# Optimization experiments

Hardware: AMD Instinct MI355X
Metric: run time of the kernel (lower is better)

## Reference

```python
import jax, jax.numpy as jnp
import numpy as np


def hard_sigmoid(x):
    # Keras hard_sigmoid: clip(0.2*x + 0.5, 0, 1)
    return jnp.clip(0.2 * x + 0.5, 0.0, 1.0)


def lstm_layer(x, W, U, b):
    """Run a Keras-style LSTM cell over time.

    x: [B, T, D], W: [D, 4H], U: [H, 4H], b: [4H]. Gate order i,f,g,o.
    Returns full hidden sequence [B, T, H].
    """
    B = x.shape[0]
    H = U.shape[0]
    h0 = jnp.zeros((B, H), dtype=x.dtype)
    c0 = jnp.zeros((B, H), dtype=x.dtype)
    # Precompute input projections for all timesteps in one big GEMM.
    xz = jnp.einsum('btd,dk->btk', x, W) + b  # [B, T, 4H]
    xz_t = jnp.swapaxes(xz, 0, 1)             # [T, B, 4H]

    def step(carry, zx_t):
        h, c = carry
        z = zx_t + h @ U                       # [B, 4H]
        i, f, g, o = jnp.split(z, 4, axis=-1)
        i = hard_sigmoid(i)
        f = hard_sigmoid(f)
        g = jnp.tanh(g)
        o = hard_sigmoid(o)
        c = f * c + i * g
        h = o * jnp.tanh(c)
        return (h, c), h

    (_, _), hs = jax.lax.scan(step, (h0, c0), xz_t)  # hs: [T, B, H]
    return jnp.swapaxes(hs, 0, 1)  # [B, T, H]


def setup_inputs() -> dict:
    key = jax.random.key(0)
    ks = jax.random.split(key, 7)
    B, T, D, H = 32, 512, 1024, 1024
    s_in = 1.0 / np.sqrt(D)
    s_h = 1.0 / np.sqrt(H)
    return {
        'x': jax.random.normal(ks[0], (B, T, D), dtype=jnp.float32),
        'W0': jax.random.normal(ks[1], (D, 4 * H), dtype=jnp.float32) * s_in,
        'U0': jax.random.normal(ks[2], (H, 4 * H), dtype=jnp.float32) * s_h,
        'b0': jnp.zeros((4 * H,), dtype=jnp.float32),
        'W1': jax.random.normal(ks[3], (H, 4 * H), dtype=jnp.float32) * s_h,
        'U1': jax.random.normal(ks[4], (H, 4 * H), dtype=jnp.float32) * s_h,
        'b1': jnp.zeros((4 * H,), dtype=jnp.float32),
    }


def reference(x, W0, U0, b0, W1, U1, b1):
    # StackedRNNCells: output of cell 0 at time t feeds cell 1 at time t.
    # Equivalent to running layer 0 over the whole sequence, then layer 1.
    h1 = lstm_layer(x, W0, U0, b0)    # [B, T, H]
    h2 = lstm_layer(h1, W1, U1, b1)   # [B, T, H]
    # RNN(return_sequences=False): last timestep output of the top cell.
    return h2[:, -1, :]
```

## Files before the change

### kernel.cpp

```cpp
#include <hip/hip_runtime.h>
#include <math.h>

#define B_  32
#define T_  512
#define H_  1024
#define G4_ 4096
#define NT  512
#define ROWP 1032
#define WROW 264

typedef __attribute__((ext_vector_type(8))) _Float16 f16x8;
typedef __attribute__((ext_vector_type(4))) float   f32x4;

__device__ __forceinline__ float hardsig(float z) {
    return fminf(fmaxf(0.2f * z + 0.5f, 0.0f), 1.0f);
}
__device__ __forceinline__ float fast_tanh(float x) {
    float ax = fabsf(x);
    float e  = __expf(-2.0f * ax);
    float t  = (1.0f - e) / (1.0f + e);
    return copysignf(t, x);
}
__device__ __forceinline__ unsigned ldA(const unsigned* p) {
    return __hip_atomic_load(p, __ATOMIC_RELAXED, __HIP_MEMORY_SCOPE_AGENT);
}
__device__ __forceinline__ void stA32(unsigned* p, unsigned v) {
    __hip_atomic_store(p, v, __ATOMIC_RELAXED, __HIP_MEMORY_SCOPE_AGENT);
}
__device__ __forceinline__ unsigned long long ldA64(const void* p) {
    return __hip_atomic_load((const unsigned long long*)p, __ATOMIC_RELAXED, __HIP_MEMORY_SCOPE_AGENT);
}
__device__ __forceinline__ void stA64(void* p, unsigned long long v) {
    __hip_atomic_store((unsigned long long*)p, v, __ATOMIC_RELAXED, __HIP_MEMORY_SCOPE_AGENT);
}
__device__ __forceinline__ float f16bits_to_f(unsigned short us) {
    _Float16 hf; __builtin_memcpy(&hf, &us, 2);
    return (float)hf;
}
__device__ __forceinline__ unsigned umin2(unsigned a, unsigned b) { return a < b ? a : b; }

__device__ __forceinline__ void load_wfrags(const float* M, int colbase, int myrow,
                                            int koff, bool keep, f16x8* wf, _Float16* st) {
    for (int kc = 0; kc < 4; ++kc) {
        __syncthreads();
        #pragma unroll
        for (int it = 0; it < 4; ++it) {
            int id  = it * NT + (int)threadIdx.x;
            int kl  = id >> 3, gc8 = id & 7;
            int gcol = (gc8 >> 1) * 1024 + colbase + (gc8 & 1) * 8;
            const float* src = M + (size_t)(kc * 256 + kl) * G4_ + gcol;
            float4 v0 = *(const float4*)src;
            float4 v1 = *(const float4*)(src + 4);
            int rb = gc8 * 8;
            st[(rb+0)*WROW+kl]=(_Float16)v0.x; st[(rb+1)*WROW+kl]=(_Float16)v0.y;
            st[(rb+2)*WROW+kl]=(_Float16)v0.z; st[(rb+3)*WROW+kl]=(_Float16)v0.w;
            st[(rb+4)*WROW+kl]=(_Float16)v1.x; st[(rb+5)*WROW+kl]=(_Float16)v1.y;
            st[(rb+6)*WROW+kl]=(_Float16)v1.z; st[(rb+7)*WROW+kl]=(_Float16)v1.w;
        }
        __syncthreads();
        if (keep) {
            #pragma unroll
            for (int kj = 0; kj < 8; ++kj)
                wf[kc*8+kj] = *(const f16x8*)&st[myrow * WROW + kj * 32 + koff];
        }
    }
    __syncthreads();
}


__global__ __launch_bounds__(NT, 1)
void lstm12(const float* __restrict__ x,
            const float* __restrict__ W0, const float* __restrict__ U0, const float* __restrict__ b0,
            const float* __restrict__ W1, const float* __restrict__ U1, const float* __restrict__ b1,
            _Float16* __restrict__ h1,
            _Float16* __restrict__ h2,
            _Float16* __restrict__ xzr,
            const _Float16* __restrict__ zp,
            unsigned* __restrict__ ctr,
            float* __restrict__ out)
{
    __shared__ __align__(16) char smem[149504];

    const int tid = threadIdx.x, bid = blockIdx.x;
    const int w = tid >> 6, l = tid & 63;
    const int koff = (l >> 4) * 8;

    if (bid >= 128) {
        _Float16* Wl = (_Float16*)smem;
        const int e = bid - 128, gbase = e * 64;
        for (int fi = tid; fi < 16384; fi += NT) {
            const int k = fi >> 4, rem = fi & 15;
            const float* src = W0 + (size_t)k * G4_ + gbase + rem * 4;
            float4 v = *(const float4*)src;
            const int kiG = k >> 5, jsub = 16 * ((k & 31) >> 3), e8 = k & 7;
            #pragma unroll
            for (int c = 0; c < 4; ++c) {
                const int j = rem * 4 + c, nf = j >> 4, lane = (j & 15) + jsub;
                float fv = (c == 0) ? v.x : (c == 1) ? v.y : (c == 2) ? v.z : v.w;
                Wl[((nf * 32 + kiG) * 64 + lane) * 8 + e8] = (_Float16)fv;
            }
        }
        float bb0[4];
        #pragma unroll
        for (int nf = 0; nf < 4; ++nf) bb0[nf] = b0[gbase + nf * 16 + (l & 15)];
        __syncthreads();

        for (int c = 0; c < 64; ++c) {
            if (c >= 4) {
                if (w == 0) {
                    const unsigned need = (unsigned)(8 * c - 24);
                    while (true) {
                        unsigned v = umin2(ldA(&ctr[2 * l]), ldA(&ctr[2 * l + 1]));
                        if (__all((int)(v >= need))) break;
                        __builtin_amdgcn_s_sleep(1);
                    }
                }
                __syncthreads();
            }

            f32x4 acc[2][4];
            #pragma unroll
            for (int p = 0; p < 2; ++p)
                #pragma unroll
                for (int nf = 0; nf < 4; ++nf) acc[p][nf] = (f32x4){0.f, 0.f, 0.f, 0.f};
            const float* xrow[2];
            #pragma unroll
            for (int p = 0; p < 2; ++p) {
                const int m = (w * 2 + p) * 16 + (l & 15);
                xrow[p] = x + ((size_t)(m & 31) * T_ + (8 * c + (m >> 5))) * 1024;
            }
            #pragma unroll 4
            for (int kiG = 0; kiG < 32; ++kiG) {
                const int kk = kiG * 32 + koff;
                f16x8 af[2];
                #pragma unroll
                for (int p = 0; p < 2; ++p) {
                    float4 v0 = *(const float4*)&xrow[p][kk];
                    float4 v1 = *(const float4*)&xrow[p][kk + 4];
                    af[p][0]=(_Float16)v0.x; af[p][1]=(_Float16)v0.y;
                    af[p][2]=(_Float16)v0.z; af[p][3]=(_Float16)v0.w;
                    af[p][4]=(_Float16)v1.x; af[p][5]=(_Float16)v1.y;
                    af[p][6]=(_Float16)v1.z; af[p][7]=(_Float16)v1.w;
                }
                #pragma unroll
                for (int nf = 0; nf < 4; ++nf) {
                    f16x8 bf = *(const f16x8*)&Wl[((nf * 32 + kiG) * 64 + l) * 8];
                    acc[0][nf] = __builtin_amdgcn_mfma_f32_16x16x32_f16(af[0], bf, acc[0][nf], 0, 0, 0);
                    acc[1][nf] = __builtin_amdgcn_mfma_f32_16x16x32_f16(af[1], bf, acc[1][nf], 0, 0, 0);
                }
            }
            #pragma unroll
            for (int p = 0; p < 2; ++p)
                #pragma unroll
                for (int nf = 0; nf < 4; ++nf)
                    #pragma unroll
                    for (int i = 0; i < 4; ++i) {
                        _Float16 hf = (_Float16)(acc[p][nf][i] + bb0[nf]);
                        unsigned short us; __builtin_memcpy(&us, &hf, 2);
                        unsigned up = us;
                        unsigned op = (unsigned)__shfl_xor((int)up, 1);
                        if (!(l & 1)) {
                            const int m = (w * 2 + p) * 16 + (l >> 4) * 4 + i;
                            size_t off = (((size_t)(c & 3) * 8 + (m >> 5)) * B_ + (m & 31)) * G4_
                                       + gbase + nf * 16 + ((l & 15) & ~1);
                            stA32((unsigned*)&xzr[off], up | (op << 16));
                        }
                    }
            asm volatile("s_waitcnt vmcnt(0)" ::: "memory");
            __syncthreads();
            if (tid == 0) stA32(&ctr[384 + e], (unsigned)(c + 1));
        }
        return;
    }

    const int dom = (bid >= 64);
    const int db  = bid & 63;
    const int jb  = db * 16;

    _Float16* stA = (_Float16*)smem;
    _Float16* stB = (_Float16*)(smem + 66048);
    float*    red = (float*)(smem + (dom ? 132096 : 66048));
    #define RED(slot, row, col) red[((slot) * 16 + (row)) * 17 + (col)]

    f16x8 wf[32];
    const int gq = w & 3;
    const int myrow = gq * 16 + (l & 15);
    if (dom == 0) {
        load_wfrags(U0, jb, myrow, koff, true, wf, stA);
    } else {
        const int rl = w >> 2;
        load_wfrags(W1, jb, myrow, koff, (rl == 0), wf, stA);
        load_wfrags(U1, jb, myrow, koff, (rl == 1), wf, stA);
    }

    const int cidx = w * 64 + l;
    const int cb = cidx >> 2, j4 = (cidx & 3) * 4;
    float creg[4] = {0.f, 0.f, 0.f, 0.f};
    float bias_[4][4];
    if (dom == 1 && w < 2) {
        #pragma unroll
        for (int g = 0; g < 4; ++g)
            #pragma unroll
            for (int c = 0; c < 4; ++c)
                bias_[g][c] = b1[(size_t)g * H_ + jb + j4 + c];
    }
    const int mt = w >> 2;
    const int rl = w >> 2;

    for (int t = 0; t < T_; ++t) {
        if (w == 0) {
            if (dom == 0) {
                const unsigned xt = (unsigned)((t >> 3) + 1);
                while (true) {
                    bool ok = (ldA(&ctr[384 + l]) >= xt);
                    if (t > 0) {
                        unsigned v0 = umin2(ldA(&ctr[2 * l]), ldA(&ctr[2 * l + 1]));
                        ok = ok && (v0 >= (unsigned)t);
                    }
                    if (__all((int)ok)) break;
                    __builtin_amdgcn_s_sleep(1);
                }
            } else {
                while (true) {
                    unsigned v0 = umin2(ldA(&ctr[2 * l]), ldA(&ctr[2 * l + 1]));
                    bool ok = (v0 >= (unsigned)(t + 1));
                    if (t > 0) {
                        unsigned v1 = umin2(ldA(&ctr[128 + 2 * l]), ldA(&ctr[128 + 2 * l + 1]));
                        ok = ok && (v1 >= (unsigned)t);
                    }
                    if (__all((int)ok)) break;
                    __builtin_amdgcn_s_sleep(1);
                }
            }
        }
        __syncthreads();

        if (dom == 0) {
            const char* src = t ? (const char*)(h1 + (size_t)(t - 1) * B_ * H_) : (const char*)zp;
            #pragma unroll
            for (int it = 0; it < 8; ++it) {
                const int fb = tid * 16 + it * 8192;
                const int row = fb >> 11, rb = fb & 2047;
                *(uint4*)&smem[row * 2064 + rb] = *(const uint4*)(src + fb);
            }
        } else {
            const char* s1 = (const char*)(h1 + (size_t)t * B_ * H_);
            const char* s2 = t ? (const char*)(h2 + (size_t)(t - 1) * B_ * H_) : (const char*)zp;
            #pragma unroll
            for (int it = 0; it < 8; ++it) {
                const int fb = tid * 16 + it * 8192;
                const int row = fb >> 11, rb = fb & 2047;
                *(uint4*)&smem[row * 2064 + rb] = *(const uint4*)(s1 + fb);
                *(uint4*)&smem[66048 + row * 2064 + rb] = *(const uint4*)(s2 + fb);
            }
        }
        unsigned long long xzq[4];
        if (dom == 0 && w < 2) {
            const size_t xbase = (((size_t)((t >> 3) & 3) * 8 + (t & 7)) * B_ + cb) * G4_ + jb + j4;
            #pragma unroll
            for (int gg = 0; gg < 4; ++gg) xzq[gg] = ldA64(&xzr[xbase + gg * 1024]);
        }
        __syncthreads();

        if (dom == 0) {
            const _Float16* ar = stA + (mt * 16 + (l & 15)) * ROWP;
            f32x4 ac0 = {0,0,0,0}, ac1 = {0,0,0,0}, ac2 = {0,0,0,0}, ac3 = {0,0,0,0};
            #pragma unroll
            for (int k = 0; k < 32; k += 4) {
                ac0 = __builtin_amdgcn_mfma_f32_16x16x32_f16(*(const f16x8*)&ar[(k+0)*32 + koff], wf[k+0], ac0, 0, 0, 0);
                ac1 = __builtin_amdgcn_mfma_f32_16x16x32_f16(*(const f16x8*)&ar[(k+1)*32 + koff], wf[k+1], ac1, 0, 0, 0);
                ac2 = __builtin_amdgcn_mfma_f32_16x16x32_f16(*(const f16x8*)&ar[(k+2)*32 + koff], wf[k+2], ac2, 0, 0, 0);
                ac3 = __builtin_amdgcn_mfma_f32_16x16x32_f16(*(const f16x8*)&ar[(k+3)*32 + koff], wf[k+3], ac3, 0, 0, 0);
            }
            f32x4 acc = (ac0 + ac1) + (ac2 + ac3);
            #pragma unroll
            for (int i = 0; i < 4; ++i)
                RED(mt * 4 + gq, (l >> 4) * 4 + i, (l & 15)) = acc[i];
        } else {
            const _Float16* ab = (rl ? stB : stA);
            const _Float16* ar0 = ab + (l & 15) * ROWP;
            const _Float16* ar1 = ab + (16 + (l & 15)) * ROWP;
            f32x4 ac0 = {0,0,0,0}, ac1 = {0,0,0,0};
            #pragma unroll
            for (int k = 0; k < 32; ++k) {
                const int kk = k * 32 + koff;
                f16x8 bfr = wf[k];
                ac0 = __builtin_amdgcn_mfma_f32_16x16x32_f16(*(const f16x8*)&ar0[kk], bfr, ac0, 0, 0, 0);
                ac1 = __builtin_amdgcn_mfma_f32_16x16x32_f16(*(const f16x8*)&ar1[kk], bfr, ac1, 0, 0, 0);
            }
            #pragma unroll
            for (int i = 0; i < 4; ++i) {
                RED(rl * 8 + 0 * 4 + gq, (l >> 4) * 4 + i, (l & 15)) = ac0[i];
                RED(rl * 8 + 1 * 4 + gq, (l >> 4) * 4 + i, (l & 15)) = ac1[i];
            }
        }
        __syncthreads();

        if (w < 2) {
            const int rmt = cb >> 4, row = cb & 15;
            unsigned long long pk = 0;
            float hv4[4];
            if (dom == 0) {
                asm volatile("s_waitcnt vmcnt(0)" ::: "memory");
                #pragma unroll
                for (int c = 0; c < 4; ++c) {
                    float z[4];
                    #pragma unroll
                    for (int gg = 0; gg < 4; ++gg) {
                        float xv = f16bits_to_f((unsigned short)((xzq[gg] >> (16 * c)) & 0xffffu));
                        z[gg] = RED(rmt * 4 + gg, row, j4 + c) + xv;
                    }
                    float ig = hardsig(z[0]), fg = hardsig(z[1]);
                    float gv = fast_tanh(z[2]), og = hardsig(z[3]);
                    creg[c] = fg * creg[c] + ig * gv;
                    hv4[c] = og * fast_tanh(creg[c]);
                    _Float16 hf = (_Float16)hv4[c];
                    unsigned short us; __builtin_memcpy(&us, &hf, 2);
                    pk |= ((unsigned long long)us) << (16 * c);
                }
                stA64(&h1[((size_t)t * B_ + cb) * H_ + jb + j4], pk);
                asm volatile("s_waitcnt vmcnt(0)" ::: "memory");
                if (l == 0) stA32(&ctr[db * 2 + w], (unsigned)(t + 1));
            } else {
                #pragma unroll
                for (int c = 0; c < 4; ++c) {
                    float z[4];
                    #pragma unroll
                    for (int gg = 0; gg < 4; ++gg)
                        z[gg] = RED(0 + rmt * 4 + gg, row, j4 + c)
                              + RED(8 + rmt * 4 + gg, row, j4 + c) + bias_[gg][c];
                    float ig = hardsig(z[0]), fg = hardsig(z[1]);
                    float gv = fast_tanh(z[2]), og = hardsig(z[3]);
                    creg[c] = fg * creg[c] + ig * gv;
                    hv4[c] = og * fast_tanh(creg[c]);
                    _Float16 hf = (_Float16)hv4[c];
                    unsigned short us; __builtin_memcpy(&us, &hf, 2);
                    pk |= ((unsigned long long)us) << (16 * c);
                }
                stA64(&h2[((size_t)t * B_ + cb) * H_ + jb + j4], pk);
                if (t == T_ - 1)
                    *(float4*)&out[(size_t)cb * H_ + jb + j4] = make_float4(hv4[0], hv4[1], hv4[2], hv4[3]);
                asm volatile("s_waitcnt vmcnt(0)" ::: "memory");
                if (l == 0) stA32(&ctr[128 + db * 2 + w], (unsigned)(t + 1));
            }
        }
    }
}

extern "C" void kernel_launch(void* const* d_in, const int* in_sizes, int n_in,
                              void* d_out, int out_size, void* d_ws, size_t ws_size,
                              hipStream_t stream) {
    const float* x  = (const float*)d_in[0];
    const float* W0 = (const float*)d_in[1];
    const float* U0 = (const float*)d_in[2];
    const float* b0 = (const float*)d_in[3];
    const float* W1 = (const float*)d_in[4];
    const float* U1 = (const float*)d_in[5];
    const float* b1 = (const float*)d_in[6];
    float* out = (float*)d_out;

    char* ws = (char*)d_ws;
    const size_t off_h1 = 0;
    const size_t off_h2 = 33554432;
    const size_t off_xz = 67108864;
    const size_t off_zp = 75497472;
    const size_t off_ct = 75563008;

    _Float16* h1  = (_Float16*)(ws + off_h1);
    _Float16* h2  = (_Float16*)(ws + off_h2);
    _Float16* xzr = (_Float16*)(ws + off_xz);
    _Float16* zp  = (_Float16*)(ws + off_zp);
    unsigned* ctr = (unsigned*)(ws + off_ct);

    hipMemsetAsync(ws + off_zp, 0, 65536 + 8192, stream);

    hipLaunchKernelGGL(lstm12, dim3(192), dim3(NT), 0, stream,
                       x, W0, U0, b0, W1, U1, b1,
                       h1, h2, xzr, zp, ctr, out);
}
```

Measured before the change: 4.195 ms.

## Replace per-step counter barriers with sentinel-polled data flags for hidden-state handoff

Instead of having each block spin on per-timestep counters before loading the previous hidden state, the h1/h2 buffers are pre-filled with 0xFF sentinels. Consumers poll the data itself until no sentinel words remain and stage it into LDS. Layer-0 counters are now published only every 8 steps, and layer-1 counters are dropped entirely. This removes a global flag round trip and the extra s_waitcnt from the recurrence critical path. The cost is a 64MB memset each call and relying on 32-bit halves of valid fp16 data never equalling 0xFFFFFFFF (a pair of fp16 NaNs).

```diff
diff --git a/kernel.cpp b/kernel.cpp
--- a/kernel.cpp
+++ b/kernel.cpp
@@ -8,6 +8,7 @@
 #define NT  512
 #define ROWP 1032
 #define WROW 264
+#define SENT 0xFFFFFFFFu
 
 typedef __attribute__((ext_vector_type(8))) _Float16 f16x8;
 typedef __attribute__((ext_vector_type(4))) float   f32x4;
@@ -38,6 +39,38 @@
     return (float)hf;
 }
 __device__ __forceinline__ unsigned umin2(unsigned a, unsigned b) { return a < b ? a : b; }
+
+__device__ __forceinline__ void stage_poll(const char* src, char* dst, int tid) {
+    unsigned long long a[8], b[8];
+    #pragma unroll
+    for (int it = 0; it < 8; ++it) {
+        const char* p = src + tid * 16 + it * 8192;
+        a[it] = ldA64(p); b[it] = ldA64(p + 8);
+    }
+    unsigned pend = 0xFFu;
+    while (true) {
+        unsigned np = 0;
+        #pragma unroll
+        for (int it = 0; it < 8; ++it)
+            if (pend & (1u << it))
+                if ((unsigned)a[it] == SENT || (unsigned)b[it] == SENT) np |= (1u << it);
+        #pragma unroll
+        for (int it = 0; it < 8; ++it)
+            if ((pend & (1u << it)) && !(np & (1u << it))) {
+                const int fb = tid * 16 + it * 8192;
+                unsigned long long* d = (unsigned long long*)(dst + (fb >> 11) * 2064 + (fb & 2047));
+                d[0] = a[it]; d[1] = b[it];
+            }
+        pend = np;
+        if (!pend) break;
+        #pragma unroll
+        for (int it = 0; it < 8; ++it)
+            if (pend & (1u << it)) {
+                const char* p = src + tid * 16 + it * 8192;
+                a[it] = ldA64(p); b[it] = ldA64(p + 8);
+            }
+    }
+}
 
 __device__ __forceinline__ void load_wfrags(const float* M, int colbase, int myrow,
                                             int koff, bool keep, f16x8* wf, _Float16* st) {
@@ -69,7 +102,7 @@
 
 
 __global__ __launch_bounds__(NT, 1)
-void lstm12(const float* __restrict__ x,
+void lstm13(const float* __restrict__ x,
             const float* __restrict__ W0, const float* __restrict__ U0, const float* __restrict__ b0,
             const float* __restrict__ W1, const float* __restrict__ U1, const float* __restrict__ b1,
             _Float16* __restrict__ h1,
@@ -117,7 +150,6 @@
                 }
                 __syncthreads();
             }
-
             f32x4 acc[2][4];
             #pragma unroll
             for (int p = 0; p < 2; ++p)
@@ -178,7 +210,6 @@
     const int jb  = db * 16;
 
     _Float16* stA = (_Float16*)smem;
-    _Float16* stB = (_Float16*)(smem + 66048);
     float*    red = (float*)(smem + (dom ? 132096 : 66048));
     #define RED(slot, row, col) red[((slot) * 16 + (row)) * 17 + (col)]
 
@@ -188,9 +219,9 @@
     if (dom == 0) {
         load_wfrags(U0, jb, myrow, koff, true, wf, stA);
     } else {
-        const int rl = w >> 2;
-        load_wfrags(W1, jb, myrow, koff, (rl == 0), wf, stA);
-        load_wfrags(U1, jb, myrow, koff, (rl == 1), wf, stA);
+        const int rl0 = w >> 2;
+        load_wfrags(W1, jb, myrow, koff, (rl0 == 0), wf, stA);
+        load_wfrags(U1, jb, myrow, koff, (rl0 == 1), wf, stA);
     }
 
     const int cidx = w * 64 + l;
@@ -207,62 +238,23 @@
     const int mt = w >> 2;
     const int rl = w >> 2;
 
-    for (int t = 0; t < T_; ++t) {
-        if (w == 0) {
-            if (dom == 0) {
+    if (dom == 0) {
+        for (int t = 0; t < T_; ++t) {
+            if (w < 2 && (t & 7) == 0) {
                 const unsigned xt = (unsigned)((t >> 3) + 1);
-                while (true) {
-                    bool ok = (ldA(&ctr[384 + l]) >= xt);
-                    if (t > 0) {
-                        unsigned v0 = umin2(ldA(&ctr[2 * l]), ldA(&ctr[2 * l + 1]));
-                        ok = ok && (v0 >= (unsigned)t);
-                    }
-                    if (__all((int)ok)) break;
-                    __builtin_amdgcn_s_sleep(1);
-                }
-            } else {
-                while (true) {
-                    unsigned v0 = umin2(ldA(&ctr[2 * l]), ldA(&ctr[2 * l + 1]));
-                    bool ok = (v0 >= (unsigned)(t + 1));
-                    if (t > 0) {
-                        unsigned v1 = umin2(ldA(&ctr[128 + 2 * l]), ldA(&ctr[128 + 2 * l + 1]));
-                        ok = ok && (v1 >= (unsigned)t);
-                    }
-                    if (__all((int)ok)) break;
-                    __builtin_amdgcn_s_sleep(1);
-                }
-            }
-        }
-        __syncthreads();
-
-        if (dom == 0) {
+                while (!__all((int)(ldA(&ctr[384 + l]) >= xt))) __builtin_amdgcn_s_sleep(1);
+                asm volatile("" ::: "memory");
+            }
             const char* src = t ? (const char*)(h1 + (size_t)(t - 1) * B_ * H_) : (const char*)zp;
-            #pragma unroll
-            for (int it = 0; it < 8; ++it) {
-                const int fb = tid * 16 + it * 8192;
-                const int row = fb >> 11, rb = fb & 2047;
-                *(uint4*)&smem[row * 2064 + rb] = *(const uint4*)(src + fb);
-            }
-        } else {
-            const char* s1 = (const char*)(h1 + (size_t)t * B_ * H_);
-            const char* s2 = t ? (const char*)(h2 + (size_t)(t - 1) * B_ * H_) : (const char*)zp;
-            #pragma unroll
-            for (int it = 0; it < 8; ++it) {
-                const int fb = tid * 16 + it * 8192;
-                const int row = fb >> 11, rb = fb & 2047;
-                *(uint4*)&smem[row * 2064 + rb] = *(const uint4*)(s1 + fb);
-                *(uint4*)&smem[66048 + row * 2064 + rb] = *(const uint4*)(s2 + fb);
-            }
-        }
-        unsigned long long xzq[4];
-        if (dom == 0 && w < 2) {
-            const size_t xbase = (((size_t)((t >> 3) & 3) * 8 + (t & 7)) * B_ + cb) * G4_ + jb + j4;
-            #pragma unroll
-            for (int gg = 0; gg < 4; ++gg) xzq[gg] = ldA64(&xzr[xbase + gg * 1024]);
-        }
-        __syncthreads();
-
-        if (dom == 0) {
+            stage_poll(src, smem, tid);
+            unsigned long long xzq[4];
+            if (w < 2) {
+                const size_t xbase = (((size_t)((t >> 3) & 3) * 8 + (t & 7)) * B_ + cb) * G4_ + jb + j4;
+                #pragma unroll
+                for (int gg = 0; gg < 4; ++gg) xzq[gg] = ldA64(&xzr[xbase + gg * 1024]);
+            }
+            __syncthreads();
+
             const _Float16* ar = stA + (mt * 16 + (l & 15)) * ROWP;
             f32x4 ac0 = {0,0,0,0}, ac1 = {0,0,0,0}, ac2 = {0,0,0,0}, ac3 = {0,0,0,0};
             #pragma unroll
@@ -276,32 +268,12 @@
             #pragma unroll
             for (int i = 0; i < 4; ++i)
                 RED(mt * 4 + gq, (l >> 4) * 4 + i, (l & 15)) = acc[i];
-        } else {
-            const _Float16* ab = (rl ? stB : stA);
-            const _Float16* ar0 = ab + (l & 15) * ROWP;
-            const _Float16* ar1 = ab + (16 + (l & 15)) * ROWP;
-            f32x4 ac0 = {0,0,0,0}, ac1 = {0,0,0,0};
-            #pragma unroll
-            for (int k = 0; k < 32; ++k) {
-                const int kk = k * 32 + koff;
-                f16x8 bfr = wf[k];
-                ac0 = __builtin_amdgcn_mfma_f32_16x16x32_f16(*(const f16x8*)&ar0[kk], bfr, ac0, 0, 0, 0);
-                ac1 = __builtin_amdgcn_mfma_f32_16x16x32_f16(*(const f16x8*)&ar1[kk], bfr, ac1, 0, 0, 0);
-            }
-            #pragma unroll
-            for (int i = 0; i < 4; ++i) {
-                RED(rl * 8 + 0 * 4 + gq, (l >> 4) * 4 + i, (l & 15)) = ac0[i];
-                RED(rl * 8 + 1 * 4 + gq, (l >> 4) * 4 + i, (l & 15)) = ac1[i];
-            }
-        }
-        __syncthreads();
-
-        if (w < 2) {
-            const int rmt = cb >> 4, row = cb & 15;
-            unsigned long long pk = 0;
-            float hv4[4];
-            if (dom == 0) {
+            __syncthreads();
+
+            if (w < 2) {
                 asm volatile("s_waitcnt vmcnt(0)" ::: "memory");
+                const int rmt = cb >> 4, row = cb & 15;
+                unsigned long long pk = 0;
                 #pragma unroll
                 for (int c = 0; c < 4; ++c) {
                     float z[4];
@@ -313,15 +285,49 @@
                     float ig = hardsig(z[0]), fg = hardsig(z[1]);
                     float gv = fast_tanh(z[2]), og = hardsig(z[3]);
                     creg[c] = fg * creg[c] + ig * gv;
-                    hv4[c] = og * fast_tanh(creg[c]);
-                    _Float16 hf = (_Float16)hv4[c];
+                    float hv = og * fast_tanh(creg[c]);
+                    _Float16 hf = (_Float16)hv;
                     unsigned short us; __builtin_memcpy(&us, &hf, 2);
                     pk |= ((unsigned long long)us) << (16 * c);
                 }
                 stA64(&h1[((size_t)t * B_ + cb) * H_ + jb + j4], pk);
-                asm volatile("s_waitcnt vmcnt(0)" ::: "memory");
-                if (l == 0) stA32(&ctr[db * 2 + w], (unsigned)(t + 1));
-            } else {
+                if ((t & 7) == 7) {
+                    asm volatile("s_waitcnt vmcnt(0)" ::: "memory");
+                    if (l == 0) stA32(&ctr[db * 2 + w], (unsigned)(t + 1));
+                }
+            }
+        }
+    } else {
+        _Float16* stB = (_Float16*)(smem + 66048);
+        for (int t = 0; t < T_; ++t) {
+            const char* s2 = t ? (const char*)(h2 + (size_t)(t - 1) * B_ * H_) : (const char*)zp;
+            stage_poll(s2, (char*)stB, tid);
+            const char* s1 = (const char*)(h1 + (size_t)t * B_ * H_);
+            stage_poll(s1, smem, tid);
+            __syncthreads();
+
+            const _Float16* ab = (rl ? stB : stA);
+            const _Float16* ar0 = ab + (l & 15) * ROWP;
+            const _Float16* ar1 = ab + (16 + (l & 15)) * ROWP;
+            f32x4 ac0 = {0,0,0,0}, ac1 = {0,0,0,0};
+            #pragma unroll
+            for (int k = 0; k < 32; ++k) {
+                const int kk = k * 32 + koff;
+                f16x8 bfr = wf[k];
+                ac0 = __builtin_amdgcn_mfma_f32_16x16x32_f16(*(const f16x8*)&ar0[kk], bfr, ac0, 0, 0, 0);
+                ac1 = __builtin_amdgcn_mfma_f32_16x16x32_f16(*(const f16x8*)&ar1[kk], bfr, ac1, 0, 0, 0);
+            }
+            #pragma unroll
+            for (int i = 0; i < 4; ++i) {
+                RED(rl * 8 + 0 * 4 + gq, (l >> 4) * 4 + i, (l & 15)) = ac0[i];
+                RED(rl * 8 + 1 * 4 + gq, (l >> 4) * 4 + i, (l & 15)) = ac1[i];
+            }
+            __syncthreads();
+
+            if (w < 2) {
+                const int rmt = cb >> 4, row = cb & 15;
+                unsigned long long pk = 0;
+                float hv4[4];
                 #pragma unroll
                 for (int c = 0; c < 4; ++c) {
                     float z[4];
@@ -340,8 +346,6 @@
                 stA64(&h2[((size_t)t * B_ + cb) * H_ + jb + j4], pk);
                 if (t == T_ - 1)
                     *(float4*)&out[(size_t)cb * H_ + jb + j4] = make_float4(hv4[0], hv4[1], hv4[2], hv4[3]);
-                asm volatile("s_waitcnt vmcnt(0)" ::: "memory");
-                if (l == 0) stA32(&ctr[128 + db * 2 + w], (unsigned)(t + 1));
             }
         }
     }
@@ -372,9 +376,10 @@
     _Float16* zp  = (_Float16*)(ws + off_zp);
     unsigned* ctr = (unsigned*)(ws + off_ct);
 
+    hipMemsetAsync(ws, 0xFF, 67108864, stream);
     hipMemsetAsync(ws + off_zp, 0, 65536 + 8192, stream);
 
-    hipLaunchKernelGGL(lstm12, dim3(192), dim3(NT), 0, stream,
+    hipLaunchKernelGGL(lstm13, dim3(192), dim3(NT), 0, stream,
                        x, W0, U0, b0, W1, U1, b1,
                        h1, h2, xzr, zp, ctr, out);
 }
```

New measurement: 4.922 ms. 17.3% more time.

## Swizzle staged h tiles into MFMA fragment layout and split per-wave waits

Applied to the files above, without the earlier changes.

The hidden-state tile staged into LDS now uses an XOR-swizzled, fragment-ordered layout instead of padded rows. Each lane can then read its MFMA A operand with one contiguous 16-byte access, with fewer bank conflicts. The single wave-0 spin followed by __syncthreads is replaced by per-wave spins, so each wave group waits only on the counters for the data it stages. In layer 2, the two wave halves now stage h1 and h2 separately, which lets one half start loading before the other half's dependency is met. The dom-0 MFMA chain shrinks from four accumulators to two.

```diff
diff --git a/kernel.cpp b/kernel.cpp
--- a/kernel.cpp
+++ b/kernel.cpp
@@ -6,7 +6,6 @@
 #define H_  1024
 #define G4_ 4096
 #define NT  512
-#define ROWP 1032
 #define WROW 264
 
 typedef __attribute__((ext_vector_type(8))) _Float16 f16x8;
@@ -38,6 +37,15 @@
     return (float)hf;
 }
 __device__ __forceinline__ unsigned umin2(unsigned a, unsigned b) { return a < b ? a : b; }
+
+__device__ __forceinline__ void stage_granule(const char* src, _Float16* dst, int fb) {
+    uint4 v = *(const uint4*)(src + fb);
+    const int r = fb >> 11, c0 = (fb & 2047) >> 1;
+    const int kiG = c0 >> 5, q = (c0 >> 3) & 3;
+    const int ln = (r & 15) + 16 * q;
+    const int pl = ln ^ ((ln >> 3) & 6) ^ (kiG & 1);
+    *(uint4*)&dst[(((r >> 4) * 32 + kiG) * 64 + pl) * 8] = v;
+}
 
 __device__ __forceinline__ void load_wfrags(const float* M, int colbase, int myrow,
                                             int koff, bool keep, f16x8* wf, _Float16* st) {
@@ -69,7 +77,7 @@
 
 
 __global__ __launch_bounds__(NT, 1)
-void lstm12(const float* __restrict__ x,
+void lstm14(const float* __restrict__ x,
             const float* __restrict__ W0, const float* __restrict__ U0, const float* __restrict__ b0,
             const float* __restrict__ W1, const float* __restrict__ U1, const float* __restrict__ b1,
             _Float16* __restrict__ h1,
@@ -79,11 +87,12 @@
             unsigned* __restrict__ ctr,
             float* __restrict__ out)
 {
-    __shared__ __align__(16) char smem[149504];
+    __shared__ __align__(16) char smem[148480];
 
     const int tid = threadIdx.x, bid = blockIdx.x;
     const int w = tid >> 6, l = tid & 63;
     const int koff = (l >> 4) * 8;
+    const int pl0 = l ^ ((l >> 3) & 6);
 
     if (bid >= 128) {
         _Float16* Wl = (_Float16*)smem;
@@ -117,7 +126,6 @@
                 }
                 __syncthreads();
             }
-
             f32x4 acc[2][4];
             #pragma unroll
             for (int p = 0; p < 2; ++p)
@@ -178,8 +186,8 @@
     const int jb  = db * 16;
 
     _Float16* stA = (_Float16*)smem;
-    _Float16* stB = (_Float16*)(smem + 66048);
-    float*    red = (float*)(smem + (dom ? 132096 : 66048));
+    _Float16* stB = (_Float16*)(smem + 65536);
+    float*    red = (float*)(smem + (dom ? 131072 : 65536));
     #define RED(slot, row, col) red[((slot) * 16 + (row)) * 17 + (col)]
 
     f16x8 wf[32];
@@ -188,9 +196,9 @@
     if (dom == 0) {
         load_wfrags(U0, jb, myrow, koff, true, wf, stA);
     } else {
-        const int rl = w >> 2;
-        load_wfrags(W1, jb, myrow, koff, (rl == 0), wf, stA);
-        load_wfrags(U1, jb, myrow, koff, (rl == 1), wf, stA);
+        const int rl0 = w >> 2;
+        load_wfrags(W1, jb, myrow, koff, (rl0 == 0), wf, stA);
+        load_wfrags(U1, jb, myrow, koff, (rl0 == 1), wf, stA);
     }
 
     const int cidx = w * 64 + l;
@@ -206,53 +214,51 @@
     }
     const int mt = w >> 2;
     const int rl = w >> 2;
+    const int wr = w & 3;
 
     for (int t = 0; t < T_; ++t) {
-        if (w == 0) {
-            if (dom == 0) {
-                const unsigned xt = (unsigned)((t >> 3) + 1);
-                while (true) {
-                    bool ok = (ldA(&ctr[384 + l]) >= xt);
-                    if (t > 0) {
-                        unsigned v0 = umin2(ldA(&ctr[2 * l]), ldA(&ctr[2 * l + 1]));
-                        ok = ok && (v0 >= (unsigned)t);
-                    }
-                    if (__all((int)ok)) break;
-                    __builtin_amdgcn_s_sleep(1);
-                }
-            } else {
+        if (dom == 0) {
+            if (t > 0) {
                 while (true) {
                     unsigned v0 = umin2(ldA(&ctr[2 * l]), ldA(&ctr[2 * l + 1]));
-                    bool ok = (v0 >= (unsigned)(t + 1));
-                    if (t > 0) {
-                        unsigned v1 = umin2(ldA(&ctr[128 + 2 * l]), ldA(&ctr[128 + 2 * l + 1]));
-                        ok = ok && (v1 >= (unsigned)t);
-                    }
-                    if (__all((int)ok)) break;
+                    if (__all((int)(v0 >= (unsigned)t))) break;
                     __builtin_amdgcn_s_sleep(1);
                 }
             }
-        }
-        __syncthreads();
+            if (w < 2) {
+                const unsigned xt = (unsigned)((t >> 3) + 1);
+                while (!__all((int)(ldA(&ctr[384 + l]) >= xt))) __builtin_amdgcn_s_sleep(1);
+            }
+        } else {
+            if (rl == 0) {
+                while (true) {
+                    unsigned v0 = umin2(ldA(&ctr[2 * l]), ldA(&ctr[2 * l + 1]));
+                    if (__all((int)(v0 >= (unsigned)(t + 1)))) break;
+                    __builtin_amdgcn_s_sleep(1);
+                }
+            } else if (t > 0) {
+                while (true) {
+                    unsigned v1 = umin2(ldA(&ctr[128 + 2 * l]), ldA(&ctr[128 + 2 * l + 1]));
+                    if (__all((int)(v1 >= (unsigned)t))) break;
+                    __builtin_amdgcn_s_sleep(1);
+                }
+            }
+        }
+        asm volatile("" ::: "memory");
 
         if (dom == 0) {
             const char* src = t ? (const char*)(h1 + (size_t)(t - 1) * B_ * H_) : (const char*)zp;
             #pragma unroll
-            for (int it = 0; it < 8; ++it) {
-                const int fb = tid * 16 + it * 8192;
-                const int row = fb >> 11, rb = fb & 2047;
-                *(uint4*)&smem[row * 2064 + rb] = *(const uint4*)(src + fb);
-            }
+            for (int it = 0; it < 8; ++it)
+                stage_granule(src, stA, tid * 16 + it * 8192);
         } else {
-            const char* s1 = (const char*)(h1 + (size_t)t * B_ * H_);
-            const char* s2 = t ? (const char*)(h2 + (size_t)(t - 1) * B_ * H_) : (const char*)zp;
-            #pragma unroll
-            for (int it = 0; it < 8; ++it) {
-                const int fb = tid * 16 + it * 8192;
-                const int row = fb >> 11, rb = fb & 2047;
-                *(uint4*)&smem[row * 2064 + rb] = *(const uint4*)(s1 + fb);
-                *(uint4*)&smem[66048 + row * 2064 + rb] = *(const uint4*)(s2 + fb);
-            }
+            const char* src = (rl == 0)
+                ? (const char*)(h1 + (size_t)t * B_ * H_)
+                : (t ? (const char*)(h2 + (size_t)(t - 1) * B_ * H_) : (const char*)zp);
+            _Float16* dst = (rl == 0) ? stA : stB;
+            #pragma unroll
+            for (int it = 0; it < 16; ++it)
+                stage_granule(src, dst, (wr * 64 + l) * 16 + it * 4096);
         }
         unsigned long long xzq[4];
         if (dom == 0 && w < 2) {
@@ -263,30 +269,29 @@
         __syncthreads();
 
         if (dom == 0) {
-            const _Float16* ar = stA + (mt * 16 + (l & 15)) * ROWP;
-            f32x4 ac0 = {0,0,0,0}, ac1 = {0,0,0,0}, ac2 = {0,0,0,0}, ac3 = {0,0,0,0};
-            #pragma unroll
-            for (int k = 0; k < 32; k += 4) {
-                ac0 = __builtin_amdgcn_mfma_f32_16x16x32_f16(*(const f16x8*)&ar[(k+0)*32 + koff], wf[k+0], ac0, 0, 0, 0);
-                ac1 = __builtin_amdgcn_mfma_f32_16x16x32_f16(*(const f16x8*)&ar[(k+1)*32 + koff], wf[k+1], ac1, 0, 0, 0);
-                ac2 = __builtin_amdgcn_mfma_f32_16x16x32_f16(*(const f16x8*)&ar[(k+2)*32 + koff], wf[k+2], ac2, 0, 0, 0);
-                ac3 = __builtin_amdgcn_mfma_f32_16x16x32_f16(*(const f16x8*)&ar[(k+3)*32 + koff], wf[k+3], ac3, 0, 0, 0);
-            }
-            f32x4 acc = (ac0 + ac1) + (ac2 + ac3);
+            f32x4 ac0 = {0,0,0,0}, ac1 = {0,0,0,0};
+            #pragma unroll
+            for (int k = 0; k < 32; k += 2) {
+                ac0 = __builtin_amdgcn_mfma_f32_16x16x32_f16(
+                    *(const f16x8*)&stA[((mt * 32 + k) * 64 + pl0) * 8], wf[k], ac0, 0, 0, 0);
+                ac1 = __builtin_amdgcn_mfma_f32_16x16x32_f16(
+                    *(const f16x8*)&stA[((mt * 32 + k + 1) * 64 + (pl0 ^ 1)) * 8], wf[k + 1], ac1, 0, 0, 0);
+            }
+            f32x4 acc = ac0 + ac1;
             #pragma unroll
             for (int i = 0; i < 4; ++i)
                 RED(mt * 4 + gq, (l >> 4) * 4 + i, (l & 15)) = acc[i];
         } else {
             const _Float16* ab = (rl ? stB : stA);
-            const _Float16* ar0 = ab + (l & 15) * ROWP;
-            const _Float16* ar1 = ab + (16 + (l & 15)) * ROWP;
             f32x4 ac0 = {0,0,0,0}, ac1 = {0,0,0,0};
             #pragma unroll
             for (int k = 0; k < 32; ++k) {
-                const int kk = k * 32 + koff;
+                const int pl = pl0 ^ (k & 1);
                 f16x8 bfr = wf[k];
-                ac0 = __builtin_amdgcn_mfma_f32_16x16x32_f16(*(const f16x8*)&ar0[kk], bfr, ac0, 0, 0, 0);
-                ac1 = __builtin_amdgcn_mfma_f32_16x16x32_f16(*(const f16x8*)&ar1[kk], bfr, ac1, 0, 0, 0);
+                ac0 = __builtin_amdgcn_mfma_f32_16x16x32_f16(
+                    *(const f16x8*)&ab[((0 * 32 + k) * 64 + pl) * 8], bfr, ac0, 0, 0, 0);
+                ac1 = __builtin_amdgcn_mfma_f32_16x16x32_f16(
+                    *(const f16x8*)&ab[((1 * 32 + k) * 64 + pl) * 8], bfr, ac1, 0, 0, 0);
             }
             #pragma unroll
             for (int i = 0; i < 4; ++i) {
@@ -374,7 +379,7 @@
 
     hipMemsetAsync(ws + off_zp, 0, 65536 + 8192, stream);
 
-    hipLaunchKernelGGL(lstm12, dim3(192), dim3(NT), 0, stream,
+    hipLaunchKernelGGL(lstm14, dim3(192), dim3(NT), 0, stream,
                        x, W0, U0, b0, W1, U1, b1,
                        h1, h2, xzr, zp, ctr, out);
 }
```

Result: slower. 6.981 ms (+66.4%).
